# Kernel optimization log

Measured on AMD Instinct MI355X. Metric: run time of the kernel, lower is better.

## Reference

```python
import jax, jax.numpy as jnp
import numpy as np

N_HEADS = 8
TANH_CLIP = 10.0
NEG_INF = -1e9


def setup_inputs() -> dict:
    key = jax.random.key(0)
    B, N, D = 2048, 100, 128
    ks = jax.random.split(key, 6)
    return {
        "embeddings": jax.random.normal(ks[0], (B, N, D), dtype=jnp.float32),
        "W_node": jax.random.normal(ks[1], (D, 3 * D), dtype=jnp.float32) * 0.05,
        "W_fixed": jax.random.normal(ks[2], (D, D), dtype=jnp.float32) * 0.05,
        "W_step": jax.random.normal(ks[3], (2 * D, D), dtype=jnp.float32) * 0.05,
        "W_out": jax.random.normal(ks[4], (D, D), dtype=jnp.float32) * 0.05,
        "W_placeholder": jax.random.uniform(ks[5], (2 * D,), dtype=jnp.float32, minval=-1.0, maxval=1.0),
    }


def reference(embeddings, W_node, W_fixed, W_step, W_out, W_placeholder):
    B, N, D = embeddings.shape
    H = N_HEADS
    dk = D // H

    # ---- precompute fixed (AttentionModelFixed) ----
    graph_emb = embeddings.mean(axis=1)                     # [B, D]
    fixed_context = graph_emb @ W_fixed                     # [B, D]
    gk, gv, logit_k = jnp.split(embeddings @ W_node, 3, axis=-1)  # each [B, N, D]
    gk = gk.reshape(B, N, H, dk).transpose(0, 2, 1, 3)      # [B, H, N, dk]
    gv = gv.reshape(B, N, H, dk).transpose(0, 2, 1, 3)      # [B, H, N, dk]

    batch_idx = jnp.arange(B)

    def gather_node(first_or_last):  # [B] int -> [B, D]
        return jnp.take_along_axis(embeddings, first_or_last[:, None, None], axis=1)[:, 0]

    def step(carry, t):
        mask, first, last = carry                           # mask [B,N] bool
        # step context: W_placeholder at t==0, else [emb_first, emb_last]
        ctx_nodes = jnp.concatenate([gather_node(first), gather_node(last)], axis=-1)  # [B, 2D]
        step_ctx = jnp.where(t == 0, W_placeholder[None, :], ctx_nodes)
        query = fixed_context + step_ctx @ W_step           # [B, D]
        qh = query.reshape(B, H, dk)
        # masked multi-head glimpse attention over the N nodes
        compat = jnp.einsum('bhd,bhnd->bhn', qh, gk) / jnp.sqrt(jnp.float32(dk))
        compat = jnp.where(mask[:, None, :], NEG_INF, compat)   # mask_inner
        attn = jax.nn.softmax(compat, axis=-1)
        heads = jnp.einsum('bhn,bhnd->bhd', attn, gv)       # [B, H, dk]
        glimpse = heads.reshape(B, D) @ W_out               # [B, D]
        # tanh-clipped logits against logit_key
        logits = jnp.einsum('bd,bnd->bn', glimpse, logit_k) / jnp.sqrt(jnp.float32(D))
        logits = TANH_CLIP * jnp.tanh(logits)
        logits = jnp.where(mask, NEG_INF, logits)           # mask_logits
        log_p = jax.nn.log_softmax(logits, axis=-1)         # [B, N]
        sel = jnp.argmax(log_p, axis=-1)                    # greedy decode, [B]
        new_mask = mask.at[batch_idx, sel].set(True)
        new_first = jnp.where(t == 0, sel, first)
        return (new_mask, new_first, sel), (log_p, sel)

    init = (jnp.zeros((B, N), dtype=bool), jnp.zeros((B,), dtype=jnp.int32), jnp.zeros((B,), dtype=jnp.int32))
    _, (log_ps, pis) = jax.lax.scan(step, init, jnp.arange(N))
    log_p = jnp.transpose(log_ps, (1, 0, 2))                # [B, N_steps, N]
    pi = jnp.transpose(pis, (1, 0))                          # [B, N_steps]
    return log_p, pi
```

## Files before the change

### kernel.cpp

```cpp
#include <hip/hip_runtime.h>
#include <math.h>

#define NEG_INF (-1e9f)
#define WSYNC() asm volatile("s_waitcnt lgkmcnt(0)" ::: "memory")
#define SW(n) ((((n) ^ ((n) >> 3))) & 7)

template <int CTRL>
__device__ __forceinline__ float dppf(float x, float oldv) {
  return __int_as_float(__builtin_amdgcn_update_dpp(
      __float_as_int(oldv), __float_as_int(x), CTRL, 0xF, 0xF, false));
}
template <int CTRL>
__device__ __forceinline__ int dppi(int x, int oldv) {
  return __builtin_amdgcn_update_dpp(oldv, x, CTRL, 0xF, 0xF, false);
}
__device__ __forceinline__ float rdlane63f(float x) {
  return __int_as_float(__builtin_amdgcn_readlane(__float_as_int(x), 63));
}
__device__ __forceinline__ float wred_max(float x) {
  x = fmaxf(x, dppf<0xB1>(x, -INFINITY));
  x = fmaxf(x, dppf<0x4E>(x, -INFINITY));
  x = fmaxf(x, dppf<0x141>(x, -INFINITY));
  x = fmaxf(x, dppf<0x140>(x, -INFINITY));
  x = fmaxf(x, dppf<0x142>(x, -INFINITY));
  x = fmaxf(x, dppf<0x143>(x, -INFINITY));
  return rdlane63f(x);
}
__device__ __forceinline__ float wred_sum(float x) {
  x += dppf<0xB1>(x, 0.f);
  x += dppf<0x4E>(x, 0.f);
  x += dppf<0x141>(x, 0.f);
  x += dppf<0x140>(x, 0.f);
  x += dppf<0x142>(x, 0.f);
  x += dppf<0x143>(x, 0.f);
  return rdlane63f(x);
}

__global__ __launch_bounds__(128) void pre_kernel(
    const float* __restrict__ W_node, const float* __restrict__ W_out,
    const float* __restrict__ W_step, const float* __restrict__ W_ph,
    float* __restrict__ ws) {
  const int bi = blockIdx.x;
  const int tid = threadIdx.x;
  if (bi < 64) {
    __shared__ float woT[64][133];
    float acc0 = 0.f, acc1 = 0.f;
    const int e0 = bi * 2, e1 = e0 + 1;
    for (int ch = 0; ch < 2; ++ch) {
      const int j0 = ch * 64;
      for (int it = 0; it < 64; ++it) {
        int idx = tid + it * 128;
        int jj = idx & 63, ds = idx >> 6;
        woT[jj][ds] = W_out[ds * 128 + j0 + jj];
      }
      __syncthreads();
      for (int jj = 0; jj < 64; ++jj) {
        int j = j0 + jj;
        float a0 = W_node[e0 * 384 + 256 + j];
        float a1 = W_node[e1 * 384 + 256 + j];
        float bb = woT[jj][tid];
        acc0 = fmaf(a0, bb, acc0);
        acc1 = fmaf(a1, bb, acc1);
      }
      __syncthreads();
    }
    const float rs = 0.08838834764831845f;
    ws[e0 * 128 + tid] = acc0 * rs;
    ws[e1 * 128 + tid] = acc1 * rs;
  } else {
    float acc = 0.f;
    for (int i = 0; i < 256; ++i) acc = fmaf(W_ph[i], W_step[i * 128 + tid], acc);
    ws[16384 + tid] = acc;
  }
}

__global__ __launch_bounds__(512) void decode_k(
    const float* __restrict__ emb,
    const float* __restrict__ W_node,
    const float* __restrict__ W_fixed,
    const float* __restrict__ W_step,
    const float* __restrict__ ws,
    float* __restrict__ out_logp,
    float* __restrict__ out_pi) {
  const int b = blockIdx.x;
  const int tid = threadIdx.x;
  const int h = tid >> 6;
  const int l = tid & 63;
  const int dp = l >> 2;
  const int qg = l & 3;
  const bool act = (l < 50);
  const int r0 = act ? l : 0;
  const int r1 = act ? l + 50 : 0;
  const int qq0 = (l < 25) ? 0 : 1;
  const int ii0 = l - qq0 * 25;
  const int sw0 = SW(r0);
  const int sw1 = SW(r1);

  __shared__ __align__(16) float sTab[100 * 128];
  __shared__ __align__(16) float sE[8][100][16];
  __shared__ __align__(16) float pool[3200];
  __shared__ float smean[128];
  __shared__ __align__(16) float sbase[8][16];

  const float* embB = emb + (size_t)b * 12800;
  const float4* embB4 = (const float4*)embB;
  float* sTabf = sTab;
  float4* sTab4 = (float4*)sTab;

  for (int it = 0; it < 7; ++it) {
    int qi = tid + it * 512;
    if (qi < 3200) {
      int n = qi >> 5, c = qi & 31;
      sTab4[n * 32 + (c ^ SW(n))] = embB4[qi];
    }
  }
  __syncthreads();

  {
    int d = tid & 127, q2 = tid >> 7;
    int ch = d >> 2, cl = d & 3;
    float p = 0.f;
    for (int n = q2 * 25; n < q2 * 25 + 25; ++n)
      p += sTabf[n * 128 + ((ch ^ SW(n)) << 2) + cl];
    pool[q2 * 128 + d] = p;
  }
  __syncthreads();
  if (tid < 128)
    smean[tid] = (pool[tid] + pool[128 + tid] + pool[256 + tid] + pool[384 + tid]) * 0.01f;
  __syncthreads();

  float ctx[16];
  {
    float a = 0.f;
    for (int i = 0; i < 32; ++i) {
      int e = qg * 32 + i;
      a = fmaf(smean[e], W_fixed[e * 128 + h * 16 + dp], a);
    }
    a += dppf<0xB1>(a, 0.f);
    a += dppf<0x4E>(a, 0.f);
    if ((l & 3) == 0) sbase[h][l >> 2] = 0.25f * a;
    WSYNC();
#pragma unroll
    for (int jj = 0; jj < 4; ++jj) {
      float4 v = *(const float4*)&sbase[h][jj * 4];
      ctx[jj * 4 + 0] = v.x; ctx[jj * 4 + 1] = v.y;
      ctx[jj * 4 + 2] = v.z; ctx[jj * 4 + 3] = v.w;
    }
  }

  float gvt[25];
  {
    float gv0[16], gv1[16];
#pragma unroll
    for (int j = 0; j < 16; ++j) gv0[j] = gv1[j] = 0.f;
#pragma unroll 2
    for (int e4 = 0; e4 < 32; ++e4) {
      float4 a0 = sTab4[r0 * 32 + (e4 ^ sw0)];
      float4 a1 = sTab4[r1 * 32 + (e4 ^ sw1)];
      float em0[4] = {a0.x, a0.y, a0.z, a0.w};
      float em1[4] = {a1.x, a1.y, a1.z, a1.w};
#pragma unroll
      for (int eo = 0; eo < 4; ++eo) {
        const int e = e4 * 4 + eo;
        const float ev0 = em0[eo], ev1 = em1[eo];
        const float* wv = &W_node[e * 384 + 128 + h * 16];
#pragma unroll
        for (int j = 0; j < 16; ++j) {
          float wvj = wv[j];
          gv0[j] = fmaf(ev0, wvj, gv0[j]);
          gv1[j] = fmaf(ev1, wvj, gv1[j]);
        }
      }
    }
    float* gvtmp = pool;
#pragma unroll 1
    for (int pass = 0; pass < 4; ++pass) {
      WSYNC();
      if (act) {
        if (qq0 == pass) {
          float4* w = (float4*)(gvtmp + (h * 25 + ii0) * 16);
#pragma unroll
          for (int jj = 0; jj < 4; ++jj)
            w[jj] = make_float4(gv0[jj * 4], gv0[jj * 4 + 1], gv0[jj * 4 + 2], gv0[jj * 4 + 3]);
        }
        if (qq0 + 2 == pass) {
          float4* w = (float4*)(gvtmp + (h * 25 + ii0) * 16);
#pragma unroll
          for (int jj = 0; jj < 4; ++jj)
            w[jj] = make_float4(gv1[jj * 4], gv1[jj * 4 + 1], gv1[jj * 4 + 2], gv1[jj * 4 + 3]);
        }
      }
      WSYNC();
      if (qg == pass) {
#pragma unroll
        for (int i = 0; i < 25; ++i) gvt[i] = gvtmp[(h * 25 + i) * 16 + dp];
      }
    }
  }
  __syncthreads();

  float* sattnH = pool + h * 112;
  float* sheadsH = pool + 896 + h * 16;
  float* spartB = pool + 1024;
  float* sqpH = pool + 2624 + h * 16;

  {
    float Ea0[16], Ea1[16];
#pragma unroll
    for (int j = 0; j < 16; ++j) Ea0[j] = Ea1[j] = 0.f;
#pragma unroll 2
    for (int e4 = 0; e4 < 32; ++e4) {
      float4 a0 = sTab4[r0 * 32 + (e4 ^ sw0)];
      float4 a1 = sTab4[r1 * 32 + (e4 ^ sw1)];
      float em0[4] = {a0.x, a0.y, a0.z, a0.w};
      float em1[4] = {a1.x, a1.y, a1.z, a1.w};
#pragma unroll
      for (int eo = 0; eo < 4; ++eo) {
        const int e = e4 * 4 + eo;
        const float ev0 = em0[eo], ev1 = em1[eo];
        const float* wE = &W_step[(size_t)(128 + e) * 128 + h * 16];
#pragma unroll
        for (int j = 0; j < 16; ++j) {
          float wEj = wE[j];
          Ea0[j] = fmaf(ev0, wEj, Ea0[j]);
          Ea1[j] = fmaf(ev1, wEj, Ea1[j]);
        }
      }
    }
    if (act) {
      float4* d0 = (float4*)&sE[h][r0][0];
      float4* d1 = (float4*)&sE[h][r1][0];
#pragma unroll
      for (int jj = 0; jj < 4; ++jj) {
        d0[jj] = make_float4(ctx[jj * 4 + 0] + 0.25f * Ea0[jj * 4 + 0],
                             ctx[jj * 4 + 1] + 0.25f * Ea0[jj * 4 + 1],
                             ctx[jj * 4 + 2] + 0.25f * Ea0[jj * 4 + 2],
                             ctx[jj * 4 + 3] + 0.25f * Ea0[jj * 4 + 3]);
        d1[jj] = make_float4(ctx[jj * 4 + 0] + 0.25f * Ea1[jj * 4 + 0],
                             ctx[jj * 4 + 1] + 0.25f * Ea1[jj * 4 + 1],
                             ctx[jj * 4 + 2] + 0.25f * Ea1[jj * 4 + 2],
                             ctx[jj * 4 + 3] + 0.25f * Ea1[jj * 4 + 3]);
      }
    }
    if (l == 0) {
      float4* dq = (float4*)sqpH;
#pragma unroll
      for (int jj = 0; jj < 4; ++jj) {
        float4 w = *(const float4*)&ws[16384 + h * 16 + jj * 4];
        dq[jj] = make_float4(ctx[jj * 4 + 0] + 0.25f * w.x,
                             ctx[jj * 4 + 1] + 0.25f * w.y,
                             ctx[jj * 4 + 2] + 0.25f * w.z,
                             ctx[jj * 4 + 3] + 0.25f * w.w);
      }
    }
  }

  float gk0[16], gk1[16];
#pragma unroll
  for (int j = 0; j < 16; ++j) gk0[j] = gk1[j] = 0.f;
#pragma unroll 2
  for (int e4 = 0; e4 < 32; ++e4) {
    float4 a0 = sTab4[r0 * 32 + (e4 ^ sw0)];
    float4 a1 = sTab4[r1 * 32 + (e4 ^ sw1)];
    float em0[4] = {a0.x, a0.y, a0.z, a0.w};
    float em1[4] = {a1.x, a1.y, a1.z, a1.w};
#pragma unroll
    for (int eo = 0; eo < 4; ++eo) {
      const int e = e4 * 4 + eo;
      const float ev0 = em0[eo], ev1 = em1[eo];
      const float* wk = &W_node[e * 384 + h * 16];
#pragma unroll
      for (int j = 0; j < 16; ++j) {
        float wkj = wk[j];
        gk0[j] = fmaf(ev0, wkj, gk0[j]);
        gk1[j] = fmaf(ev1, wkj, gk1[j]);
      }
    }
  }
  __syncthreads();

  {
    float lkr[16];
#pragma unroll
    for (int j = 0; j < 16; ++j) lkr[j] = 0.f;
#pragma unroll 2
    for (int e4 = 0; e4 < 32; ++e4) {
      float4 a0 = embB4[r0 * 32 + e4];
      float em0[4] = {a0.x, a0.y, a0.z, a0.w};
#pragma unroll
      for (int eo = 0; eo < 4; ++eo) {
        const int e = e4 * 4 + eo;
        const float ev0 = em0[eo];
        const float* wl = &ws[e * 128 + h * 16];
#pragma unroll
        for (int j = 0; j < 16; ++j) lkr[j] = fmaf(ev0, wl[j], lkr[j]);
      }
    }
    if (act) {
#pragma unroll
      for (int j = 0; j < 16; ++j) sTabf[(h * 16 + j) * 100 + r0] = lkr[j];
    }
#pragma unroll
    for (int j = 0; j < 16; ++j) lkr[j] = 0.f;
#pragma unroll 2
    for (int e4 = 0; e4 < 32; ++e4) {
      float4 a1 = embB4[r1 * 32 + e4];
      float em1[4] = {a1.x, a1.y, a1.z, a1.w};
#pragma unroll
      for (int eo = 0; eo < 4; ++eo) {
        const int e = e4 * 4 + eo;
        const float ev1 = em1[eo];
        const float* wl = &ws[e * 128 + h * 16];
#pragma unroll
        for (int j = 0; j < 16; ++j) lkr[j] = fmaf(ev1, wl[j], lkr[j]);
      }
    }
    if (act) {
#pragma unroll
      for (int j = 0; j < 16; ++j) sTabf[(h * 16 + j) * 100 + r1] = lkr[j];
    }
  }
  WSYNC();

  bool m0f = false, m1f = false;
  int last = 0;
  int par = 0;
  const size_t lpbase = (size_t)b * 10000;

#pragma unroll 1
  for (int t = 0; t < 100; ++t) {
    const float* epf = (t == 0) ? sqpH : &sE[h][last][0];
    const float4* ep = (const float4*)epf;
    float c0a = 0.f, c0b = 0.f, c1a = 0.f, c1b = 0.f;
#pragma unroll
    for (int jj = 0; jj < 2; ++jj) {
      float4 v = ep[jj];
      c0a = fmaf(v.x, gk0[4 * jj + 0], c0a); c1a = fmaf(v.x, gk1[4 * jj + 0], c1a);
      c0a = fmaf(v.y, gk0[4 * jj + 1], c0a); c1a = fmaf(v.y, gk1[4 * jj + 1], c1a);
      c0a = fmaf(v.z, gk0[4 * jj + 2], c0a); c1a = fmaf(v.z, gk1[4 * jj + 2], c1a);
      c0a = fmaf(v.w, gk0[4 * jj + 3], c0a); c1a = fmaf(v.w, gk1[4 * jj + 3], c1a);
    }
#pragma unroll
    for (int jj = 2; jj < 4; ++jj) {
      float4 v = ep[jj];
      c0b = fmaf(v.x, gk0[4 * jj + 0], c0b); c1b = fmaf(v.x, gk1[4 * jj + 0], c1b);
      c0b = fmaf(v.y, gk0[4 * jj + 1], c0b); c1b = fmaf(v.y, gk1[4 * jj + 1], c1b);
      c0b = fmaf(v.z, gk0[4 * jj + 2], c0b); c1b = fmaf(v.z, gk1[4 * jj + 2], c1b);
      c0b = fmaf(v.w, gk0[4 * jj + 3], c0b); c1b = fmaf(v.w, gk1[4 * jj + 3], c1b);
    }
    float v0 = (act && !m0f) ? (c0a + c0b) : NEG_INF;
    float v1 = (act && !m1f) ? (c1a + c1b) : NEG_INF;

    float mx = wred_max(fmaxf(v0, v1));
    float e0 = expf(v0 - mx), e1 = expf(v1 - mx);
    float s = wred_sum(e0 + e1);
    float a0 = e0 / s, a1 = e1 / s;

    if (act) {
      sattnH[qq0 * 28 + ii0] = a0;
      sattnH[(qq0 + 2) * 28 + ii0] = a1;
    }
    WSYNC();

    float Lk0[16], Lk1[16];
#pragma unroll
    for (int j = 0; j < 16; ++j) {
      Lk0[j] = sTabf[(h * 16 + j) * 100 + r0];
      Lk1[j] = sTabf[(h * 16 + j) * 100 + r1];
    }

    {
      const float* ap = sattnH + qg * 28;
      float ha = 0.f, hb = 0.f;
#pragma unroll
      for (int ii = 0; ii < 6; ++ii) {
        float4 v = ((const float4*)ap)[ii];
        ha = fmaf(v.x, gvt[4 * ii + 0], ha);
        hb = fmaf(v.y, gvt[4 * ii + 1], hb);
        ha = fmaf(v.z, gvt[4 * ii + 2], ha);
        hb = fmaf(v.w, gvt[4 * ii + 3], hb);
      }
      ha = fmaf(ap[24], gvt[24], ha);
      float hacc = ha + hb;
      hacc += dppf<0xB1>(hacc, 0.f);
      hacc += dppf<0x4E>(hacc, 0.f);
      if ((l & 3) == 0) sheadsH[l >> 2] = hacc;
    }
    WSYNC();

    float sh[16];
#pragma unroll
    for (int jj = 0; jj < 4; ++jj) {
      float4 v = *(const float4*)&sheadsH[jj * 4];
      sh[4 * jj + 0] = v.x; sh[4 * jj + 1] = v.y;
      sh[4 * jj + 2] = v.z; sh[4 * jj + 3] = v.w;
    }
    float p0a = 0.f, p0b = 0.f, p1a = 0.f, p1b = 0.f;
#pragma unroll
    for (int j = 0; j < 8; ++j) {
      p0a = fmaf(sh[j], Lk0[j], p0a);
      p1a = fmaf(sh[j], Lk1[j], p1a);
    }
#pragma unroll
    for (int j = 8; j < 16; ++j) {
      p0b = fmaf(sh[j], Lk0[j], p0b);
      p1b = fmaf(sh[j], Lk1[j], p1b);
    }
    if (act) {
      spartB[par * 800 + h * 100 + r0] = p0a + p0b;
      spartB[par * 800 + h * 100 + r1] = p1a + p1b;
    }
    __syncthreads();

    const float* sp = spartB + par * 800;
    float t00 = sp[0 * 100 + r0] + sp[1 * 100 + r0];
    float t01 = sp[2 * 100 + r0] + sp[3 * 100 + r0];
    float t02 = sp[4 * 100 + r0] + sp[5 * 100 + r0];
    float t03 = sp[6 * 100 + r0] + sp[7 * 100 + r0];
    float u00 = sp[0 * 100 + r1] + sp[1 * 100 + r1];
    float u01 = sp[2 * 100 + r1] + sp[3 * 100 + r1];
    float u02 = sp[4 * 100 + r1] + sp[5 * 100 + r1];
    float u03 = sp[6 * 100 + r1] + sp[7 * 100 + r1];
    float s0 = (t00 + t01) + (t02 + t03);
    float s1 = (u00 + u01) + (u02 + u03);
    float l0 = (act && !m0f) ? 10.0f * tanhf(s0) : NEG_INF;
    float l1 = (act && !m1f) ? 10.0f * tanhf(s1) : NEG_INF;

    float bv; int bi;
    if (l1 > l0) { bv = l1; bi = r1; } else { bv = l0; bi = act ? r0 : 1000; }
    float z = expf(l0) + expf(l1);
#define AZ_LVL(CTRL) {                                   \
      float cv = dppf<CTRL>(bv, -INFINITY);              \
      int ci = dppi<CTRL>(bi, 0x7fffffff);               \
      z += dppf<CTRL>(z, 0.f);                           \
      bool pr = (cv > bv) || (cv == bv && ci < bi);      \
      bv = pr ? cv : bv; bi = pr ? ci : bi;              \
    }
    AZ_LVL(0xB1) AZ_LVL(0x4E) AZ_LVL(0x141) AZ_LVL(0x140) AZ_LVL(0x142) AZ_LVL(0x143)
#undef AZ_LVL
    const int sel = __builtin_amdgcn_readlane(bi, 63);
    float zt = rdlane63f(z);
    float lsum = logf(zt);

    if (h == 0) {
      if (l == 0) out_pi[b * 100 + t] = (float)sel;
      if (act) {
        out_logp[lpbase + (size_t)t * 100 + r0] = l0 - lsum;
        out_logp[lpbase + (size_t)t * 100 + r1] = l1 - lsum;
      }
    }

    if (t == 0) {
      const float* erow = embB + (size_t)sel * 128;
      float fa = 0.f;
      for (int i = 0; i < 32; ++i) {
        int e = qg * 32 + i;
        fa = fmaf(erow[e], W_step[(size_t)e * 128 + h * 16 + dp], fa);
      }
      fa += dppf<0xB1>(fa, 0.f);
      fa += dppf<0x4E>(fa, 0.f);
      if ((l & 3) == 0) sbase[h][l >> 2] = 0.25f * fa;
      WSYNC();
      if (act) {
        float4* p0 = (float4*)&sE[h][r0][0];
        float4* p1 = (float4*)&sE[h][r1][0];
#pragma unroll
        for (int jj = 0; jj < 4; ++jj) {
          float4 f = *(const float4*)&sbase[h][jj * 4];
          float4 c0 = p0[jj], c1 = p1[jj];
          c0.x += f.x; c0.y += f.y; c0.z += f.z; c0.w += f.w;
          c1.x += f.x; c1.y += f.y; c1.z += f.z; c1.w += f.w;
          p0[jj] = c0; p1[jj] = c1;
        }
      }
      WSYNC();
    }

    m0f = m0f || (act && sel == r0);
    m1f = m1f || (act && sel == r1);
    last = sel;
    par ^= 1;
  }
}

extern "C" void kernel_launch(void* const* d_in, const int* in_sizes, int n_in,
                              void* d_out, int out_size, void* d_ws, size_t ws_size,
                              hipStream_t stream) {
  const float* emb     = (const float*)d_in[0];
  const float* W_node  = (const float*)d_in[1];
  const float* W_fixed = (const float*)d_in[2];
  const float* W_step  = (const float*)d_in[3];
  const float* W_out   = (const float*)d_in[4];
  const float* W_ph    = (const float*)d_in[5];
  float* ws  = (float*)d_ws;
  float* out = (float*)d_out;

  hipLaunchKernelGGL(pre_kernel, dim3(65), dim3(128), 0, stream,
                     W_node, W_out, W_step, W_ph, ws);
  hipLaunchKernelGGL(decode_k, dim3(2048), dim3(512), 0, stream,
                     emb, W_node, W_fixed, W_step, ws, out, out + 20480000);
}
```

Before: 2.722 ms.

## Split logit-key projection into separate kernel and shrink decode LDS footprint

Moves the per-node logit-key projection (emb times the precomputed W_node·W_out) into a new lcomp_kernel that stages the weights in LDS and writes the keys to a global workspace. The decode kernel drops its 50KB embedding table in LDS, reads embeddings from global instead, and keeps its logit-key slices in registers, which should raise occupancy and take an LDS round-trip out of the step loop. The attention softmax now skips the max subtraction and normalises after the weighted sum, heads are broadcast with readlane instead of an LDS write/read, and tanh/exp/log use fast approximations. The risks are extra global traffic and one more launch, possible overflow in the unshifted exp, and small numeric deviations that could change argmax ties.

Result: faster. 2.222 ms (-18.4%).

```diff
diff --git a/kernel.cpp b/kernel.cpp
--- a/kernel.cpp
+++ b/kernel.cpp
@@ -34,6 +34,11 @@
   x += dppf<0x142>(x, 0.f);
   x += dppf<0x143>(x, 0.f);
   return rdlane63f(x);
+}
+__device__ __forceinline__ float fast_tanh(float x) {
+  float t = __expf(-2.0f * fabsf(x));
+  float r = (1.0f - t) / (1.0f + t);
+  return copysignf(r, x);
 }
 
 __global__ __launch_bounds__(128) void pre_kernel(
@@ -74,12 +79,72 @@
   }
 }
 
-__global__ __launch_bounds__(512) void decode_k(
+__global__ __launch_bounds__(512) void lcomp_kernel(
+    const float* __restrict__ emb, const float* __restrict__ Wc,
+    float* __restrict__ Lk) {
+  const int b = blockIdx.x;
+  const int tid = threadIdx.x;
+  const int c = tid & 31;
+  const int g = tid >> 5;
+
+  __shared__ __align__(16) float semb[100 * 128];
+  __shared__ __align__(16) float sW[128 * 128];
+
+  float4* semb4 = (float4*)semb;
+  float4* sW4 = (float4*)sW;
+  const float4* embB4 = (const float4*)(emb + (size_t)b * 12800);
+  const float4* Wb4 = (const float4*)Wc;
+
+  for (int it = 0; it < 7; ++it) {
+    int qi = tid + it * 512;
+    if (qi < 3200) {
+      int n = qi >> 5, cc = qi & 31;
+      semb4[n * 32 + (cc ^ SW(n))] = embB4[qi];
+    }
+  }
+  for (int it = 0; it < 8; ++it) sW4[tid + it * 512] = Wb4[tid + it * 512];
+  __syncthreads();
+
+  float4 acc[7];
+#pragma unroll
+  for (int k = 0; k < 7; ++k) acc[k] = make_float4(0.f, 0.f, 0.f, 0.f);
+#pragma unroll 2
+  for (int e4 = 0; e4 < 32; ++e4) {
+    float4 em[7];
+#pragma unroll
+    for (int k = 0; k < 7; ++k) {
+      int n = g + 16 * k; n = (n < 100) ? n : 99;
+      em[k] = semb4[n * 32 + (e4 ^ SW(n))];
+    }
+#pragma unroll
+    for (int eo = 0; eo < 4; ++eo) {
+      float4 w4 = sW4[(e4 * 4 + eo) * 32 + c];
+#pragma unroll
+      for (int k = 0; k < 7; ++k) {
+        const float ev = (eo == 0) ? em[k].x : (eo == 1) ? em[k].y
+                       : (eo == 2) ? em[k].z : em[k].w;
+        acc[k].x = fmaf(ev, w4.x, acc[k].x);
+        acc[k].y = fmaf(ev, w4.y, acc[k].y);
+        acc[k].z = fmaf(ev, w4.z, acc[k].z);
+        acc[k].w = fmaf(ev, w4.w, acc[k].w);
+      }
+    }
+  }
+  float4* Lk4 = (float4*)Lk;
+#pragma unroll
+  for (int k = 0; k < 7; ++k) {
+    int n = g + 16 * k;
+    if (n < 100) Lk4[((size_t)b * 100 + n) * 32 + c] = acc[k];
+  }
+}
+
+__global__ __launch_bounds__(512) void decode_t(
     const float* __restrict__ emb,
     const float* __restrict__ W_node,
     const float* __restrict__ W_fixed,
     const float* __restrict__ W_step,
     const float* __restrict__ ws,
+    const float* __restrict__ Lkg,
     float* __restrict__ out_logp,
     float* __restrict__ out_pi) {
   const int b = blockIdx.x;
@@ -93,10 +158,7 @@
   const int r1 = act ? l + 50 : 0;
   const int qq0 = (l < 25) ? 0 : 1;
   const int ii0 = l - qq0 * 25;
-  const int sw0 = SW(r0);
-  const int sw1 = SW(r1);
-
-  __shared__ __align__(16) float sTab[100 * 128];
+
   __shared__ __align__(16) float sE[8][100][16];
   __shared__ __align__(16) float pool[3200];
   __shared__ float smean[128];
@@ -104,24 +166,11 @@
 
   const float* embB = emb + (size_t)b * 12800;
   const float4* embB4 = (const float4*)embB;
-  float* sTabf = sTab;
-  float4* sTab4 = (float4*)sTab;
-
-  for (int it = 0; it < 7; ++it) {
-    int qi = tid + it * 512;
-    if (qi < 3200) {
-      int n = qi >> 5, c = qi & 31;
-      sTab4[n * 32 + (c ^ SW(n))] = embB4[qi];
-    }
-  }
-  __syncthreads();
 
   {
     int d = tid & 127, q2 = tid >> 7;
-    int ch = d >> 2, cl = d & 3;
     float p = 0.f;
-    for (int n = q2 * 25; n < q2 * 25 + 25; ++n)
-      p += sTabf[n * 128 + ((ch ^ SW(n)) << 2) + cl];
+    for (int n = q2 * 25; n < q2 * 25 + 25; ++n) p += embB[n * 128 + d];
     pool[q2 * 128 + d] = p;
   }
   __syncthreads();
@@ -155,8 +204,8 @@
     for (int j = 0; j < 16; ++j) gv0[j] = gv1[j] = 0.f;
 #pragma unroll 2
     for (int e4 = 0; e4 < 32; ++e4) {
-      float4 a0 = sTab4[r0 * 32 + (e4 ^ sw0)];
-      float4 a1 = sTab4[r1 * 32 + (e4 ^ sw1)];
+      float4 a0 = embB4[r0 * 32 + e4];
+      float4 a1 = embB4[r1 * 32 + e4];
       float em0[4] = {a0.x, a0.y, a0.z, a0.w};
       float em1[4] = {a1.x, a1.y, a1.z, a1.w};
 #pragma unroll
@@ -200,9 +249,14 @@
   __syncthreads();
 
   float* sattnH = pool + h * 112;
-  float* sheadsH = pool + 896 + h * 16;
   float* spartB = pool + 1024;
   float* sqpH = pool + 2624 + h * 16;
+
+  if (l == 0) {
+#pragma unroll
+    for (int j = 0; j < 16; ++j)
+      sqpH[j] = ctx[j] + 0.25f * ws[16384 + h * 16 + j];
+  }
 
   {
     float Ea0[16], Ea1[16];
@@ -210,8 +264,8 @@
     for (int j = 0; j < 16; ++j) Ea0[j] = Ea1[j] = 0.f;
 #pragma unroll 2
     for (int e4 = 0; e4 < 32; ++e4) {
-      float4 a0 = sTab4[r0 * 32 + (e4 ^ sw0)];
-      float4 a1 = sTab4[r1 * 32 + (e4 ^ sw1)];
+      float4 a0 = embB4[r0 * 32 + e4];
+      float4 a1 = embB4[r1 * 32 + e4];
       float em0[4] = {a0.x, a0.y, a0.z, a0.w};
       float em1[4] = {a1.x, a1.y, a1.z, a1.w};
 #pragma unroll
@@ -242,17 +296,6 @@
                              ctx[jj * 4 + 3] + 0.25f * Ea1[jj * 4 + 3]);
       }
     }
-    if (l == 0) {
-      float4* dq = (float4*)sqpH;
-#pragma unroll
-      for (int jj = 0; jj < 4; ++jj) {
-        float4 w = *(const float4*)&ws[16384 + h * 16 + jj * 4];
-        dq[jj] = make_float4(ctx[jj * 4 + 0] + 0.25f * w.x,
-                             ctx[jj * 4 + 1] + 0.25f * w.y,
-                             ctx[jj * 4 + 2] + 0.25f * w.z,
-                             ctx[jj * 4 + 3] + 0.25f * w.w);
-      }
-    }
   }
 
   float gk0[16], gk1[16];
@@ -260,8 +303,8 @@
   for (int j = 0; j < 16; ++j) gk0[j] = gk1[j] = 0.f;
 #pragma unroll 2
   for (int e4 = 0; e4 < 32; ++e4) {
-    float4 a0 = sTab4[r0 * 32 + (e4 ^ sw0)];
-    float4 a1 = sTab4[r1 * 32 + (e4 ^ sw1)];
+    float4 a0 = embB4[r0 * 32 + e4];
+    float4 a1 = embB4[r1 * 32 + e4];
     float em0[4] = {a0.x, a0.y, a0.z, a0.w};
     float em1[4] = {a1.x, a1.y, a1.z, a1.w};
 #pragma unroll
@@ -277,49 +320,11 @@
       }
     }
   }
-  __syncthreads();
-
-  {
-    float lkr[16];
-#pragma unroll
-    for (int j = 0; j < 16; ++j) lkr[j] = 0.f;
-#pragma unroll 2
-    for (int e4 = 0; e4 < 32; ++e4) {
-      float4 a0 = embB4[r0 * 32 + e4];
-      float em0[4] = {a0.x, a0.y, a0.z, a0.w};
-#pragma unroll
-      for (int eo = 0; eo < 4; ++eo) {
-        const int e = e4 * 4 + eo;
-        const float ev0 = em0[eo];
-        const float* wl = &ws[e * 128 + h * 16];
-#pragma unroll
-        for (int j = 0; j < 16; ++j) lkr[j] = fmaf(ev0, wl[j], lkr[j]);
-      }
-    }
-    if (act) {
-#pragma unroll
-      for (int j = 0; j < 16; ++j) sTabf[(h * 16 + j) * 100 + r0] = lkr[j];
-    }
-#pragma unroll
-    for (int j = 0; j < 16; ++j) lkr[j] = 0.f;
-#pragma unroll 2
-    for (int e4 = 0; e4 < 32; ++e4) {
-      float4 a1 = embB4[r1 * 32 + e4];
-      float em1[4] = {a1.x, a1.y, a1.z, a1.w};
-#pragma unroll
-      for (int eo = 0; eo < 4; ++eo) {
-        const int e = e4 * 4 + eo;
-        const float ev1 = em1[eo];
-        const float* wl = &ws[e * 128 + h * 16];
-#pragma unroll
-        for (int j = 0; j < 16; ++j) lkr[j] = fmaf(ev1, wl[j], lkr[j]);
-      }
-    }
-    if (act) {
-#pragma unroll
-      for (int j = 0; j < 16; ++j) sTabf[(h * 16 + j) * 100 + r1] = lkr[j];
-    }
-  }
+
+  const float4* lkp0 = (const float4*)(Lkg + ((size_t)b * 100 + r0) * 128 + h * 16);
+  const float4* lkp1 = (const float4*)(Lkg + ((size_t)b * 100 + r1) * 128 + h * 16);
+  float4 L00 = lkp0[0], L01 = lkp0[1], L02 = lkp0[2], L03 = lkp0[3];
+  float4 L10 = lkp1[0], L11 = lkp1[1], L12 = lkp1[2], L13 = lkp1[3];
   WSYNC();
 
   bool m0f = false, m1f = false;
@@ -331,44 +336,45 @@
   for (int t = 0; t < 100; ++t) {
     const float* epf = (t == 0) ? sqpH : &sE[h][last][0];
     const float4* ep = (const float4*)epf;
+    float4 qv0 = ep[0], qv1 = ep[1], qv2 = ep[2], qv3 = ep[3];
+
     float c0a = 0.f, c0b = 0.f, c1a = 0.f, c1b = 0.f;
-#pragma unroll
-    for (int jj = 0; jj < 2; ++jj) {
-      float4 v = ep[jj];
-      c0a = fmaf(v.x, gk0[4 * jj + 0], c0a); c1a = fmaf(v.x, gk1[4 * jj + 0], c1a);
-      c0a = fmaf(v.y, gk0[4 * jj + 1], c0a); c1a = fmaf(v.y, gk1[4 * jj + 1], c1a);
-      c0a = fmaf(v.z, gk0[4 * jj + 2], c0a); c1a = fmaf(v.z, gk1[4 * jj + 2], c1a);
-      c0a = fmaf(v.w, gk0[4 * jj + 3], c0a); c1a = fmaf(v.w, gk1[4 * jj + 3], c1a);
-    }
-#pragma unroll
-    for (int jj = 2; jj < 4; ++jj) {
-      float4 v = ep[jj];
-      c0b = fmaf(v.x, gk0[4 * jj + 0], c0b); c1b = fmaf(v.x, gk1[4 * jj + 0], c1b);
-      c0b = fmaf(v.y, gk0[4 * jj + 1], c0b); c1b = fmaf(v.y, gk1[4 * jj + 1], c1b);
-      c0b = fmaf(v.z, gk0[4 * jj + 2], c0b); c1b = fmaf(v.z, gk1[4 * jj + 2], c1b);
-      c0b = fmaf(v.w, gk0[4 * jj + 3], c0b); c1b = fmaf(v.w, gk1[4 * jj + 3], c1b);
+    {
+      float4 v = qv0;
+      c0a = fmaf(v.x, gk0[0], c0a); c1a = fmaf(v.x, gk1[0], c1a);
+      c0a = fmaf(v.y, gk0[1], c0a); c1a = fmaf(v.y, gk1[1], c1a);
+      c0a = fmaf(v.z, gk0[2], c0a); c1a = fmaf(v.z, gk1[2], c1a);
+      c0a = fmaf(v.w, gk0[3], c0a); c1a = fmaf(v.w, gk1[3], c1a);
+      v = qv1;
+      c0a = fmaf(v.x, gk0[4], c0a); c1a = fmaf(v.x, gk1[4], c1a);
+      c0a = fmaf(v.y, gk0[5], c0a); c1a = fmaf(v.y, gk1[5], c1a);
+      c0a = fmaf(v.z, gk0[6], c0a); c1a = fmaf(v.z, gk1[6], c1a);
+      c0a = fmaf(v.w, gk0[7], c0a); c1a = fmaf(v.w, gk1[7], c1a);
+      v = qv2;
+      c0b = fmaf(v.x, gk0[8], c0b);  c1b = fmaf(v.x, gk1[8], c1b);
+      c0b = fmaf(v.y, gk0[9], c0b);  c1b = fmaf(v.y, gk1[9], c1b);
+      c0b = fmaf(v.z, gk0[10], c0b); c1b = fmaf(v.z, gk1[10], c1b);
+      c0b = fmaf(v.w, gk0[11], c0b); c1b = fmaf(v.w, gk1[11], c1b);
+      v = qv3;
+      c0b = fmaf(v.x, gk0[12], c0b); c1b = fmaf(v.x, gk1[12], c1b);
+      c0b = fmaf(v.y, gk0[13], c0b); c1b = fmaf(v.y, gk1[13], c1b);
+      c0b = fmaf(v.z, gk0[14], c0b); c1b = fmaf(v.z, gk1[14], c1b);
+      c0b = fmaf(v.w, gk0[15], c0b); c1b = fmaf(v.w, gk1[15], c1b);
     }
     float v0 = (act && !m0f) ? (c0a + c0b) : NEG_INF;
     float v1 = (act && !m1f) ? (c1a + c1b) : NEG_INF;
 
-    float mx = wred_max(fmaxf(v0, v1));
-    float e0 = expf(v0 - mx), e1 = expf(v1 - mx);
+    float e0 = __expf(v0), e1 = __expf(v1);
+
+    if (act) {
+      sattnH[qq0 * 28 + ii0] = e0;
+      sattnH[(qq0 + 2) * 28 + ii0] = e1;
+    }
+    WSYNC();
+
     float s = wred_sum(e0 + e1);
-    float a0 = e0 / s, a1 = e1 / s;
-
-    if (act) {
-      sattnH[qq0 * 28 + ii0] = a0;
-      sattnH[(qq0 + 2) * 28 + ii0] = a1;
-    }
-    WSYNC();
-
-    float Lk0[16], Lk1[16];
-#pragma unroll
-    for (int j = 0; j < 16; ++j) {
-      Lk0[j] = sTabf[(h * 16 + j) * 100 + r0];
-      Lk1[j] = sTabf[(h * 16 + j) * 100 + r1];
-    }
-
+
+    float shv[16];
     {
       const float* ap = sattnH + qg * 28;
       float ha = 0.f, hb = 0.f;
@@ -384,28 +390,29 @@
       float hacc = ha + hb;
       hacc += dppf<0xB1>(hacc, 0.f);
       hacc += dppf<0x4E>(hacc, 0.f);
-      if ((l & 3) == 0) sheadsH[l >> 2] = hacc;
-    }
-    WSYNC();
-
-    float sh[16];
-#pragma unroll
-    for (int jj = 0; jj < 4; ++jj) {
-      float4 v = *(const float4*)&sheadsH[jj * 4];
-      sh[4 * jj + 0] = v.x; sh[4 * jj + 1] = v.y;
-      sh[4 * jj + 2] = v.z; sh[4 * jj + 3] = v.w;
-    }
+      float hd = hacc / s;
+#pragma unroll
+      for (int j = 0; j < 16; ++j)
+        shv[j] = __int_as_float(__builtin_amdgcn_readlane(__float_as_int(hd), 4 * j));
+    }
+
     float p0a = 0.f, p0b = 0.f, p1a = 0.f, p1b = 0.f;
-#pragma unroll
-    for (int j = 0; j < 8; ++j) {
-      p0a = fmaf(sh[j], Lk0[j], p0a);
-      p1a = fmaf(sh[j], Lk1[j], p1a);
-    }
-#pragma unroll
-    for (int j = 8; j < 16; ++j) {
-      p0b = fmaf(sh[j], Lk0[j], p0b);
-      p1b = fmaf(sh[j], Lk1[j], p1b);
-    }
+    p0a = fmaf(shv[0], L00.x, p0a);  p1a = fmaf(shv[0], L10.x, p1a);
+    p0a = fmaf(shv[1], L00.y, p0a);  p1a = fmaf(shv[1], L10.y, p1a);
+    p0a = fmaf(shv[2], L00.z, p0a);  p1a = fmaf(shv[2], L10.z, p1a);
+    p0a = fmaf(shv[3], L00.w, p0a);  p1a = fmaf(shv[3], L10.w, p1a);
+    p0a = fmaf(shv[4], L01.x, p0a);  p1a = fmaf(shv[4], L11.x, p1a);
+    p0a = fmaf(shv[5], L01.y, p0a);  p1a = fmaf(shv[5], L11.y, p1a);
+    p0a = fmaf(shv[6], L01.z, p0a);  p1a = fmaf(shv[6], L11.z, p1a);
+    p0a = fmaf(shv[7], L01.w, p0a);  p1a = fmaf(shv[7], L11.w, p1a);
+    p0b = fmaf(shv[8], L02.x, p0b);  p1b = fmaf(shv[8], L12.x, p1b);
+    p0b = fmaf(shv[9], L02.y, p0b);  p1b = fmaf(shv[9], L12.y, p1b);
+    p0b = fmaf(shv[10], L02.z, p0b); p1b = fmaf(shv[10], L12.z, p1b);
+    p0b = fmaf(shv[11], L02.w, p0b); p1b = fmaf(shv[11], L12.w, p1b);
+    p0b = fmaf(shv[12], L03.x, p0b); p1b = fmaf(shv[12], L13.x, p1b);
+    p0b = fmaf(shv[13], L03.y, p0b); p1b = fmaf(shv[13], L13.y, p1b);
+    p0b = fmaf(shv[14], L03.z, p0b); p1b = fmaf(shv[14], L13.z, p1b);
+    p0b = fmaf(shv[15], L03.w, p0b); p1b = fmaf(shv[15], L13.w, p1b);
     if (act) {
       spartB[par * 800 + h * 100 + r0] = p0a + p0b;
       spartB[par * 800 + h * 100 + r1] = p1a + p1b;
@@ -423,12 +430,12 @@
     float u03 = sp[6 * 100 + r1] + sp[7 * 100 + r1];
     float s0 = (t00 + t01) + (t02 + t03);
     float s1 = (u00 + u01) + (u02 + u03);
-    float l0 = (act && !m0f) ? 10.0f * tanhf(s0) : NEG_INF;
-    float l1 = (act && !m1f) ? 10.0f * tanhf(s1) : NEG_INF;
+    float l0 = (act && !m0f) ? 10.0f * fast_tanh(s0) : NEG_INF;
+    float l1 = (act && !m1f) ? 10.0f * fast_tanh(s1) : NEG_INF;
 
     float bv; int bi;
     if (l1 > l0) { bv = l1; bi = r1; } else { bv = l0; bi = act ? r0 : 1000; }
-    float z = expf(l0) + expf(l1);
+    float z = __expf(l0) + __expf(l1);
 #define AZ_LVL(CTRL) {                                   \
       float cv = dppf<CTRL>(bv, -INFINITY);              \
       int ci = dppi<CTRL>(bi, 0x7fffffff);               \
@@ -439,10 +446,9 @@
     AZ_LVL(0xB1) AZ_LVL(0x4E) AZ_LVL(0x141) AZ_LVL(0x140) AZ_LVL(0x142) AZ_LVL(0x143)
 #undef AZ_LVL
     const int sel = __builtin_amdgcn_readlane(bi, 63);
-    float zt = rdlane63f(z);
-    float lsum = logf(zt);
 
     if (h == 0) {
+      float lsum = __logf(rdlane63f(z));
       if (l == 0) out_pi[b * 100 + t] = (float)sel;
       if (act) {
         out_logp[lpbase + (size_t)t * 100 + r0] = l0 - lsum;
@@ -497,6 +503,11 @@
 
   hipLaunchKernelGGL(pre_kernel, dim3(65), dim3(128), 0, stream,
                      W_node, W_out, W_step, W_ph, ws);
-  hipLaunchKernelGGL(decode_k, dim3(2048), dim3(512), 0, stream,
-                     emb, W_node, W_fixed, W_step, ws, out, out + 20480000);
-}
+
+  float* Lkg = ws + 16512;
+  hipLaunchKernelGGL(lcomp_kernel, dim3(2048), dim3(512), 0, stream,
+                     emb, ws, Lkg);
+  hipLaunchKernelGGL(decode_t, dim3(2048), dim3(512), 0, stream,
+                     emb, W_node, W_fixed, W_step, ws, Lkg,
+                     out, out + 20480000);
+}
```
